# Kernel tuning notes

Hardware: AMD Instinct MI355X
Metric: run time of the kernel (lower is better)

Reference implementation:

```python
import sys
import jax, jax.numpy as jnp
import numpy as np

sys.setrecursionlimit(100000)

MARGIN = 200.0
SAME_MARGIN = 0.0
REL_MARGIN = MARGIN - SAME_MARGIN  # margin - same_margin


def km_algorithm(mp):
    """Faithful numpy port of the repo's recursive Kuhn-Munkres (host-side,
    exactly mirroring the original CPU round-trip). mp: (n, n) float64.
    Returns transport plan T with T[link[y], y] = 1/n for matched pairs."""
    n = mp.shape[0]
    link = np.full(n, -1, dtype=np.int64)
    lx = mp.max(axis=1).astype(np.float64).copy()
    ly = np.zeros(n, dtype=np.float64)
    st = {}

    def dfs(x):
        st['visx'][x] = True
        for y in range(n):
            if st['visy'][y]:
                continue
            tmp = lx[x] + ly[y] - mp[x, y]
            if abs(tmp) < 1e-5:
                st['visy'][y] = True
                if link[y] == -1 or dfs(link[y]):
                    link[y] = x
                    return True
            elif st['sla'][y] + 1e-5 > tmp:
                st['sla'][y] = tmp
        return False

    for x in range(n):
        st['sla'] = np.full(n, 1e10, dtype=np.float64)
        while True:
            st['visx'] = np.zeros(n, dtype=bool)
            st['visy'] = np.zeros(n, dtype=bool)
            if dfs(x):
                break
            d = st['sla'][~st['visy']].min()
            lx[st['visx']] -= d
            ly[st['visy']] += d
            st['sla'][~st['visy']] -= d
    T = np.zeros((n, n), dtype=np.float64)
    for i in range(n):
        if link[i] != -1:
            T[link[i], i] = 1.0 / n
    return T


def sim_label(l1, l2):
    # (n, n) float: 1 where labels equal
    return (l1[:, None] == l2[None, :]).astype(jnp.float32)


def ground_metric(f1, f2, sim):
    # pairwise squared euclidean distances: ||a||^2 - 2 a.b + ||b||^2
    sq1 = jnp.sum(f1 * f1, axis=1)[:, None]
    sq2 = jnp.sum(f2 * f2, axis=1)[None, :]
    d2 = sq1 - 2.0 * (f1 @ f2.T) + sq2
    hinge_gm = jnp.maximum(0.0, SAME_MARGIN + REL_MARGIN - d2)   # negative pairs
    same_gm = jnp.maximum(0.0, d2 - SAME_MARGIN)                 # positive pairs
    return sim * same_gm + (1.0 - sim) * hinge_gm                # mode='both'


def setup_inputs() -> dict:
    key = jax.random.key(0)
    k1, k2, k3, k4 = jax.random.split(key, 4)
    n, d = 128, 8192
    return {
        "inputs_batch1": jax.random.normal(k1, (n, d), dtype=jnp.float32),
        "inputs_batch2": jax.random.normal(k2, (n, d), dtype=jnp.float32),
        "targets_batch1": jax.random.randint(k3, (n,), 0, 16, dtype=jnp.int64) if jax.config.jax_enable_x64 else jax.random.randint(k3, (n,), 0, 16).astype(jnp.int32),
        "targets_batch2": jax.random.randint(k4, (n,), 0, 16, dtype=jnp.int64) if jax.config.jax_enable_x64 else jax.random.randint(k4, (n,), 0, 16).astype(jnp.int32),
    }


def reference(inputs_batch1, inputs_batch2, targets_batch1, targets_batch2):
    sim = sim_label(targets_batch1, targets_batch2)
    GM = ground_metric(inputs_batch1, inputs_batch2, sim)
    # host round-trip for KM assignment, as in the original module
    T = km_algorithm(np.asarray(jax.device_get(GM), dtype=np.float64))
    T = jnp.asarray(T, dtype=jnp.float32)
    loss = jnp.sum(GM * T)
    return loss
```

## Files before the change

### kernel.cpp

```cpp
#include <hip/hip_runtime.h>

#define N 128
#define DIM 8192
#define NN (N * N)
#define ZS 128
#define NW 16
#define GSTRIDE 130

__device__ __forceinline__ void wave_fence() {
    __threadfence_block();
    __builtin_amdgcn_wave_barrier();
}
__device__ __forceinline__ double embed_key(double v, int j) {
    long long b = __double_as_longlong(v);
    return __longlong_as_double((b & ~127LL) | (long long)j);
}

__global__ __launch_bounds__(256) void d2_partial(const float* __restrict__ A,
                                                  const float* __restrict__ B,
                                                  float* __restrict__ d2p) {
    __shared__ float As[64][68];
    __shared__ float Bk[64][68];
    const int tid = threadIdx.x;
    const int b = blockIdx.x;
    const int bi = b & 1, bj = (b >> 1) & 1, bz = b >> 2;
    const int row0 = bi * 64, col0 = bj * 64, k0 = bz * 64;

    #pragma unroll
    for (int s = 0; s < 4; ++s) {
        int e = tid + s * 256;
        int r = e >> 4, q = e & 15;
        *(float4*)&As[r][q * 4] = *(const float4*)&A[(row0 + r) * DIM + k0 + q * 4];
    }
    #pragma unroll
    for (int s = 0; s < 4; ++s) {
        int e = tid + s * 256;
        int c = e & 63, kq = e >> 6;
        float4 b4 = *(const float4*)&B[(col0 + c) * DIM + k0 + kq * 4];
        Bk[kq * 4 + 0][c] = b4.x;
        Bk[kq * 4 + 1][c] = b4.y;
        Bk[kq * 4 + 2][c] = b4.z;
        Bk[kq * 4 + 3][c] = b4.w;
    }
    __syncthreads();

    const int tx = tid & 15, ty = tid >> 4;
    float acc[4][4] = {};
    #pragma unroll
    for (int kk = 0; kk < 64; kk += 4) {
        float a[4][4], bb[4][4];
        #pragma unroll
        for (int i = 0; i < 4; ++i)
            *(float4*)a[i] = *(const float4*)&As[4 * ty + i][kk];
        #pragma unroll
        for (int q = 0; q < 4; ++q)
            *(float4*)bb[q] = *(const float4*)&Bk[kk + q][4 * tx];
        #pragma unroll
        for (int i = 0; i < 4; ++i)
            #pragma unroll
            for (int q = 0; q < 4; ++q) {
                float av = a[i][q];
                #pragma unroll
                for (int j = 0; j < 4; ++j) {
                    float d = av - bb[q][j];
                    acc[i][j] = fmaf(d, d, acc[i][j]);
                }
            }
    }
    float* dst = d2p + b * 4096;
    #pragma unroll
    for (int i = 0; i < 4; ++i)
        *(float4*)&dst[(4 * ty + i) * 64 + 4 * tx] = *(float4*)acc[i];
}

__global__ __launch_bounds__(256) void reduce_gm(const float* __restrict__ d2p,
                                                 const int* __restrict__ t1,
                                                 const int* __restrict__ t2,
                                                 float* __restrict__ gm,
                                                 int* __restrict__ flagarr) {
    __shared__ int bf;
    if (threadIdx.x == 0) bf = 0;
    __syncthreads();
    const int o = blockIdx.x * 256 + threadIdx.x;
    const int i = o >> 7, j = o & 127;
    const int tilebase = (((j >> 6) << 1) | (i >> 6)) * 4096;
    const int inner = (i & 63) * 64 + (j & 63);
    const float* p = d2p + tilebase + inner;
    float s0 = 0.f, s1 = 0.f, s2 = 0.f, s3 = 0.f, s4 = 0.f, s5 = 0.f, s6 = 0.f, s7 = 0.f;
    #pragma unroll
    for (int z = 0; z < ZS; z += 8) {
        s0 += p[(z + 0) * 16384]; s1 += p[(z + 1) * 16384];
        s2 += p[(z + 2) * 16384]; s3 += p[(z + 3) * 16384];
        s4 += p[(z + 4) * 16384]; s5 += p[(z + 5) * 16384];
        s6 += p[(z + 6) * 16384]; s7 += p[(z + 7) * 16384];
    }
    float s = ((s0 + s1) + (s2 + s3)) + ((s4 + s5) + (s6 + s7));
    const int l1 = t1[i], l2 = t2[j];
    const bool same = (l1 == l2);
    float g = same ? fmaxf(s, 0.f) : fmaxf(200.f - s, 0.f);
    gm[o] = g;
    bool bad = (!same && g > 0.f) || l1 < 0 || l1 > 63 || l2 < 0 || l2 > 63;
    unsigned long long m = __ballot(bad);
    if ((threadIdx.x & 63) == 0 && m) atomicOr(&bf, 1);
    __syncthreads();
    if (threadIdx.x == 0) flagarr[blockIdx.x] = bf;
}

__global__ __launch_bounds__(1024) void solve_kernel(const float* __restrict__ gm,
                                                     const int* __restrict__ flagarr,
                                                     const int* __restrict__ t1,
                                                     const int* __restrict__ t2,
                                                     float* __restrict__ out) {
    __shared__ float gml[N * GSTRIDE];
    __shared__ int lbl1[N], lbl2[N];
    __shared__ int rowlist[N], collist[N];
    __shared__ int rcnt[64], ccnt[64], rstart[65], cstart[65], rcur[64], ccur[64];
    __shared__ int tasks[65], bigtasks[65];
    __shared__ int ntasks_s, nbig_s, flag_s;
    __shared__ double totals[NW];
    __shared__ int claimw[NW][64];
    __shared__ double ub[N + 1], vbp[N + 1], minvb[N + 1];
    __shared__ int pb[N + 1], wayb[N + 1], usedb[N + 1];
    __shared__ double redv[NW];
    __shared__ int redi[NW];
    __shared__ double big_total;
    __shared__ int jfin_s;

    const int tid = threadIdx.x;
    if (tid < 64) { rcnt[tid] = 0; ccnt[tid] = 0; rcur[tid] = 0; ccur[tid] = 0; }
    if (tid == 0) { ntasks_s = 0; nbig_s = 0; flag_s = 0; big_total = 0.0; }
    if (tid < N)  { lbl1[tid] = t1[tid]; lbl2[tid] = t2[tid]; }
    __syncthreads();
    if (tid < 64 && flagarr[tid]) atomicOr(&flag_s, 1);
    if (tid < N) {
        atomicAdd(&rcnt[lbl1[tid] & 63], 1);
        atomicAdd(&ccnt[lbl2[tid] & 63], 1);
    }
    __syncthreads();
    if (tid < 64) {
        int rs_ = rcnt[tid], cs_ = ccnt[tid];
        #pragma unroll
        for (int o = 1; o < 64; o <<= 1) {
            int tr = __shfl_up(rs_, o, 64);
            int tc = __shfl_up(cs_, o, 64);
            if (tid >= o) { rs_ += tr; cs_ += tc; }
        }
        rstart[tid + 1] = rs_;
        cstart[tid + 1] = cs_;
        if (tid == 0) { rstart[0] = 0; cstart[0] = 0; }
        if (!flag_s) {
            int R = rcnt[tid], C = ccnt[tid];
            bool valid = (R > 0) && (C > 0);
            bool small = valid && (R <= 64) && (C <= 64);
            bool big   = valid && !small;
            unsigned long long ms = __ballot(small);
            unsigned long long mb = __ballot(big);
            if (small) tasks[__popcll(ms & ((1ull << tid) - 1))] = tid;
            if (big)   bigtasks[__popcll(mb & ((1ull << tid) - 1))] = tid;
            if (tid == 0) { ntasks_s = __popcll(ms); nbig_s = __popcll(mb); }
        } else if (tid == 0) { ntasks_s = 0; nbig_s = 1; bigtasks[0] = -1; }
    }
    __syncthreads();
    if (tid < N) {
        int l1 = lbl1[tid] & 63;
        int p = atomicAdd(&rcur[l1], 1);
        rowlist[rstart[l1] + p] = tid;
        int l2 = lbl2[tid] & 63;
        int q = atomicAdd(&ccur[l2], 1);
        collist[cstart[l2] + q] = tid;
    }
    __syncthreads();
    #pragma unroll
    for (int pch = 0; pch < 16; ++pch) {
        int e = tid + pch * 1024;
        int i = e >> 7, j = e & 127;
        gml[i * GSTRIDE + j] = gm[rowlist[i] * N + collist[j]];
    }
    __syncthreads();

    const int w = tid >> 6, lane = tid & 63;
    const int ntasks = ntasks_s;
    double acc = 0.0;

    for (int tk = w; tk < ntasks; tk += NW) {
        const int c = tasks[tk];
        const int Rn = rcnt[c], Cn = ccnt[c], rs = rstart[c], cs = cstart[c];
        const bool T  = (Rn > Cn);
        const int n_  = T ? Cn : Rn;
        const int m_  = T ? Rn : Cn;
        const int rstep = T ? 1 : GSTRIDE;
        const int cstep = T ? GSTRIDE : 1;
        const int rb00 = T ? cs : rs * GSTRIDE;
        const int ob00 = T ? rs * GSTRIDE : cs;
        int* clm = claimw[w];

        const bool cA = (lane < m_), rA = (lane < n_);
        const int myoff = ob00 + lane * cstep;
        const int myrb  = rb00 + lane * rstep;

        double u = 0.0;
        if (rA) {
            float mx = 0.f;
            int a = myrb + ob00;
            for (int j = 0; j < m_; ++j) { mx = fmaxf(mx, gml[a]); a += cstep; }
            u = -(double)mx;
        }
        double v = 1e30;
        {
            int a = rb00 + myoff;
            for (int i = 0; i < n_; ++i) {
                double ui = __shfl(u, i, 64);
                if (cA) v = fmin(v, -(double)gml[a] - ui);
                a += rstep;
            }
        }
        if (cA) clm[lane] = 0x7fffffff;
        wave_fence();
        int jc = -1;
        {
            int a = myrb + ob00;
            for (int j = 0; j < m_; ++j) {
                double vj = __shfl(v, j, 64);
                if (rA && jc < 0) {
                    double s = -(double)gml[a] - u - vj;
                    if (s < 1e-7) jc = j;
                }
                a += cstep;
            }
        }
        if (rA && jc >= 0) atomicMin(&clm[jc], lane);
        wave_fence();
        int p = -1;
        if (cA && clm[lane] != 0x7fffffff) p = clm[lane];
        bool rowm = (rA && jc >= 0 && clm[jc] == lane);

        for (int ir = 0; ir < n_; ++ir) {
            if (__shfl(rowm ? 1 : 0, ir, 64)) continue;
            double minv = 1e30, markD = -1.0, ent = -1.0;
            bool used = false; int way = -2;
            if (rA && lane == ir) ent = 0.0;
            double D = 0.0;
            int i0 = ir, jprev = -1;
            int guard = 2 * m_ + 8;
            while (guard-- > 0) {
                double ui = __shfl(u, i0, 64);
                int rb = rb00 + i0 * rstep;
                if (cA && !used) {
                    double cand = D - ui - (double)gml[rb + myoff] - v;
                    if (cand < minv) { minv = cand; way = jprev; }
                }
                double kd = (cA && !used) ? embed_key(minv, lane) : 1e30;
                #pragma unroll
                for (int o = 1; o < 64; o <<= 1) kd = fmin(kd, __shfl_xor(kd, o, 64));
                long long kb = __double_as_longlong(kd);
                int j1 = (int)(kb & 127);
                double Dn = __longlong_as_double(kb & ~127LL);
                if (Dn > 1e29) break;
                D = Dn;
                int i1 = __shfl(p, j1, 64);
                if (i1 < 0) {
                    int jj = j1;
                    while (true) {
                        int wp = __shfl(way, jj, 64);
                        int pn = (wp < 0) ? ir : __shfl(p, wp, 64);
                        if (cA && lane == jj) p = pn;
                        if (wp < 0) break;
                        jj = wp;
                    }
                    if (rA && lane == ir) rowm = true;
                    break;
                }
                if (cA && lane == j1) { used = true; markD = D; }
                if (rA && lane == i1) ent = D;
                jprev = j1; i0 = i1;
            }
            if (rA && ent   >= 0.0) u += D - ent;
            if (cA && markD >= 0.0) v -= D - markD;
        }

        double val = 0.0;
        if (cA && p >= 0) val = (double)gml[rb00 + p * rstep + myoff];
        #pragma unroll
        for (int o = 1; o < 64; o <<= 1) val += __shfl_xor(val, o, 64);
        acc += val;
    }
    if (lane == 0) totals[w] = acc;
    __syncthreads();

    const int nbig = nbig_s;
    for (int bt = 0; bt < nbig; ++bt) {
        const int c = bigtasks[bt];
        int Rn, Cn, rs, cs;
        if (c < 0) { Rn = N; Cn = N; rs = 0; cs = 0; }
        else { Rn = rcnt[c]; Cn = ccnt[c]; rs = rstart[c]; cs = cstart[c]; }
        const bool T = (Rn > Cn);
        const int n_ = T ? Cn : Rn, m_ = T ? Rn : Cn;
        const int rstep = T ? 1 : GSTRIDE;
        const int cstep = T ? GSTRIDE : 1;
        const int rb00 = T ? cs : rs * GSTRIDE;
        const int ob00 = T ? rs * GSTRIDE : cs;
        auto cost = [&](int i, int j) -> double {
            return -(double)gml[rb00 + i * rstep + ob00 + j * cstep];
        };
        for (int x = tid; x <= m_; x += 1024) { vbp[x] = 0.0; pb[x] = 0; }
        for (int x = tid; x <= n_; x += 1024) { ub[x] = 0.0; }
        __syncthreads();
        for (int i = 1; i <= n_; ++i) {
            if (tid == 0) pb[0] = i;
            for (int x = tid; x <= m_; x += 1024) { minvb[x] = 1e300; usedb[x] = 0; }
            __syncthreads();
            int j0 = 0;
            int guard = 2 * m_ + 8;
            while (guard-- > 0) {
                if (tid == 0) usedb[j0] = 1;
                __syncthreads();
                const int i0 = pb[j0];
                double dl = 1e300; int jl = 0;
                if (tid < m_) {
                    int j = tid + 1;
                    if (!usedb[j]) {
                        double cur = cost(i0 - 1, j - 1) - ub[i0] - vbp[j];
                        if (cur < minvb[j]) { minvb[j] = cur; wayb[j] = j0; }
                        dl = minvb[j]; jl = j;
                    }
                }
                double rv = dl; int ri = jl;
                #pragma unroll
                for (int o = 32; o > 0; o >>= 1) {
                    double ov = __shfl_down(rv, o, 64);
                    int oi2 = __shfl_down(ri, o, 64);
                    if (ov < rv) { rv = ov; ri = oi2; }
                }
                if ((tid & 63) == 0) { redv[tid >> 6] = rv; redi[tid >> 6] = ri; }
                __syncthreads();
                if (tid == 0) {
                    double bd = 1e300; int bj = 0;
                    for (int q = 0; q < NW; ++q) if (redv[q] < bd) { bd = redv[q]; bj = redi[q]; }
                    redv[0] = bd; redi[0] = bj;
                }
                __syncthreads();
                const double delta = redv[0];
                const int j1 = redi[0];
                if (tid < m_) {
                    int j = tid + 1;
                    if (usedb[j]) { ub[pb[j]] += delta; vbp[j] -= delta; }
                    else          { minvb[j] -= delta; }
                }
                if (tid == 0) ub[pb[0]] += delta;
                __syncthreads();
                j0 = j1;
                if (pb[j0] == 0) break;
            }
            if (tid == 0) jfin_s = j0;
            __syncthreads();
            if (tid == 0) {
                int jj = jfin_s;
                while (jj) { int jp = wayb[jj]; pb[jj] = pb[jp]; jj = jp; }
            }
            __syncthreads();
        }
        double bl = 0.0;
        if (tid < m_) { int j = tid + 1; if (pb[j] != 0) bl = -cost(pb[j] - 1, j - 1); }
        #pragma unroll
        for (int o = 32; o > 0; o >>= 1) bl += __shfl_down(bl, o, 64);
        if ((tid & 63) == 0) redv[tid >> 6] = bl;
        __syncthreads();
        if (tid == 0) { double s = 0; for (int q = 0; q < NW; ++q) s += redv[q]; big_total += s; }
        __syncthreads();
    }

    if (tid == 0) {
        double s = big_total;
        for (int i = 0; i < NW; ++i) s += totals[i];
        out[0] = (float)(s / (double)N);
    }
}

extern "C" void kernel_launch(void* const* d_in, const int* in_sizes, int n_in,
                              void* d_out, int out_size, void* d_ws, size_t ws_size,
                              hipStream_t stream) {
    const float* A  = (const float*)d_in[0];
    const float* B  = (const float*)d_in[1];
    const int*   t1 = (const int*)d_in[2];
    const int*   t2 = (const int*)d_in[3];
    float* out = (float*)d_out;
    float* d2p = (float*)d_ws;
    float* gm  = (float*)d_ws + ZS * 4 * 4096;
    int*   flagarr = (int*)(gm + NN);

    d2_partial<<<ZS * 4, 256, 0, stream>>>(A, B, d2p);
    reduce_gm<<<64, 256, 0, stream>>>(d2p, t1, t2, gm, flagarr);
    solve_kernel<<<1, 1024, 0, stream>>>(gm, flagarr, t1, t2, out);
}
```

Baseline: 92.40 us.

## Split z-reduction across more threads and write label-permuted GM from reduce kernel

The reduce kernel now uses 1024 threads per block and splits the 128-slice partial-sum reduction four ways, combining the pieces through shared memory. This raises memory-level parallelism in the global reads. It also computes each row's and column's position in label-sorted order and writes GM directly in that permuted layout. The single-block solve kernel then loads it with contiguous float4 reads instead of a gather through row and column lists. The cost is that every reduce block redundantly recomputes the label counts and sorted positions, including an O(n) counting loop per thread.

```diff
diff --git a/kernel.cpp b/kernel.cpp
--- a/kernel.cpp
+++ b/kernel.cpp
@@ -73,48 +73,89 @@
         *(float4*)&dst[(4 * ty + i) * 64 + 4 * tx] = *(float4*)acc[i];
 }
 
-__global__ __launch_bounds__(256) void reduce_gm(const float* __restrict__ d2p,
-                                                 const int* __restrict__ t1,
-                                                 const int* __restrict__ t2,
-                                                 float* __restrict__ gm,
-                                                 int* __restrict__ flagarr) {
+__global__ __launch_bounds__(1024) void reduce_gm(const float* __restrict__ d2p,
+                                                  const int* __restrict__ t1,
+                                                  const int* __restrict__ t2,
+                                                  float* __restrict__ gmp,
+                                                  int* __restrict__ flagarr) {
+    __shared__ int l1o[N], l2o[N], l1c[N], l2c[N];
+    __shared__ int rc[64], cc[64], rst[64], cst[64];
+    __shared__ int rpos[N], cpos[N];
+    __shared__ float psum[3][256];
     __shared__ int bf;
-    if (threadIdx.x == 0) bf = 0;
-    __syncthreads();
-    const int o = blockIdx.x * 256 + threadIdx.x;
+    const int tid = threadIdx.x;
+    if (tid == 0) bf = 0;
+    if (tid < 64) { rc[tid] = 0; cc[tid] = 0; }
+    if (tid < N) {
+        int a = t1[tid], b = t2[tid];
+        l1o[tid] = a; l2o[tid] = b; l1c[tid] = a & 63; l2c[tid] = b & 63;
+    }
+    __syncthreads();
+    if (tid < N) {
+        atomicAdd(&rc[l1c[tid]], 1);
+        atomicAdd(&cc[l2c[tid]], 1);
+        if (l1o[tid] < 0 || l1o[tid] > 63 || l2o[tid] < 0 || l2o[tid] > 63) atomicOr(&bf, 1);
+    }
+    __syncthreads();
+    if (tid < 64) {
+        int rs_ = rc[tid], cs_ = cc[tid];
+        #pragma unroll
+        for (int o = 1; o < 64; o <<= 1) {
+            int tr = __shfl_up(rs_, o, 64);
+            int tc = __shfl_up(cs_, o, 64);
+            if (tid >= o) { rs_ += tr; cs_ += tc; }
+        }
+        rst[tid] = rs_ - rc[tid];
+        cst[tid] = cs_ - cc[tid];
+    }
+    __syncthreads();
+    if (tid < N) {
+        int cr = 0, L = l1c[tid];
+        int cq = 0, M = l2c[tid];
+        for (int k = 0; k < tid; ++k) {
+            cr += (l1c[k] == L);
+            cq += (l2c[k] == M);
+        }
+        rpos[tid] = rst[L] + cr;
+        cpos[tid] = cst[M] + cq;
+    }
+    __syncthreads();
+
+    const int oo = tid & 255, zq = tid >> 8;
+    const int o = blockIdx.x * 256 + oo;
     const int i = o >> 7, j = o & 127;
-    const int tilebase = (((j >> 6) << 1) | (i >> 6)) * 4096;
-    const int inner = (i & 63) * 64 + (j & 63);
-    const float* p = d2p + tilebase + inner;
+    const int tb = (((j >> 6) << 1) | (i >> 6)) * 4096;
+    const float* p = d2p + tb + (i & 63) * 64 + (j & 63) + zq * 32 * 16384;
     float s0 = 0.f, s1 = 0.f, s2 = 0.f, s3 = 0.f, s4 = 0.f, s5 = 0.f, s6 = 0.f, s7 = 0.f;
     #pragma unroll
-    for (int z = 0; z < ZS; z += 8) {
+    for (int z = 0; z < 32; z += 8) {
         s0 += p[(z + 0) * 16384]; s1 += p[(z + 1) * 16384];
         s2 += p[(z + 2) * 16384]; s3 += p[(z + 3) * 16384];
         s4 += p[(z + 4) * 16384]; s5 += p[(z + 5) * 16384];
         s6 += p[(z + 6) * 16384]; s7 += p[(z + 7) * 16384];
     }
     float s = ((s0 + s1) + (s2 + s3)) + ((s4 + s5) + (s6 + s7));
-    const int l1 = t1[i], l2 = t2[j];
-    const bool same = (l1 == l2);
-    float g = same ? fmaxf(s, 0.f) : fmaxf(200.f - s, 0.f);
-    gm[o] = g;
-    bool bad = (!same && g > 0.f) || l1 < 0 || l1 > 63 || l2 < 0 || l2 > 63;
-    unsigned long long m = __ballot(bad);
-    if ((threadIdx.x & 63) == 0 && m) atomicOr(&bf, 1);
-    __syncthreads();
-    if (threadIdx.x == 0) flagarr[blockIdx.x] = bf;
-}
-
-__global__ __launch_bounds__(1024) void solve_kernel(const float* __restrict__ gm,
+    if (zq) psum[zq - 1][oo] = s;
+    __syncthreads();
+    if (zq == 0) {
+        s += psum[0][oo] + psum[1][oo] + psum[2][oo];
+        const bool same = (l1o[i] == l2o[j]);
+        float g = same ? fmaxf(s, 0.f) : fmaxf(200.f - s, 0.f);
+        gmp[rpos[i] * N + cpos[j]] = g;
+        if (!same && g > 0.f) atomicOr(&bf, 1);
+    }
+    __syncthreads();
+    if (tid == 0) flagarr[blockIdx.x] = bf;
+}
+
+__global__ __launch_bounds__(1024) void solve_kernel(const float* __restrict__ gmp,
                                                      const int* __restrict__ flagarr,
                                                      const int* __restrict__ t1,
                                                      const int* __restrict__ t2,
                                                      float* __restrict__ out) {
     __shared__ float gml[N * GSTRIDE];
     __shared__ int lbl1[N], lbl2[N];
-    __shared__ int rowlist[N], collist[N];
-    __shared__ int rcnt[64], ccnt[64], rstart[65], cstart[65], rcur[64], ccur[64];
+    __shared__ int rcnt[64], ccnt[64], rstart[65], cstart[65];
     __shared__ int tasks[65], bigtasks[65];
     __shared__ int ntasks_s, nbig_s, flag_s;
     __shared__ double totals[NW];
@@ -127,7 +168,15 @@
     __shared__ int jfin_s;
 
     const int tid = threadIdx.x;
-    if (tid < 64) { rcnt[tid] = 0; ccnt[tid] = 0; rcur[tid] = 0; ccur[tid] = 0; }
+    #pragma unroll
+    for (int pch = 0; pch < 4; ++pch) {
+        int e = (tid + pch * 1024) * 4;
+        int i = e >> 7, j = e & 127;
+        float4 v4 = *(const float4*)&gmp[e];
+        *(float2*)&gml[i * GSTRIDE + j]     = make_float2(v4.x, v4.y);
+        *(float2*)&gml[i * GSTRIDE + j + 2] = make_float2(v4.z, v4.w);
+    }
+    if (tid < 64) { rcnt[tid] = 0; ccnt[tid] = 0; }
     if (tid == 0) { ntasks_s = 0; nbig_s = 0; flag_s = 0; big_total = 0.0; }
     if (tid < N)  { lbl1[tid] = t1[tid]; lbl2[tid] = t2[tid]; }
     __syncthreads();
@@ -159,22 +208,6 @@
             if (big)   bigtasks[__popcll(mb & ((1ull << tid) - 1))] = tid;
             if (tid == 0) { ntasks_s = __popcll(ms); nbig_s = __popcll(mb); }
         } else if (tid == 0) { ntasks_s = 0; nbig_s = 1; bigtasks[0] = -1; }
-    }
-    __syncthreads();
-    if (tid < N) {
-        int l1 = lbl1[tid] & 63;
-        int p = atomicAdd(&rcur[l1], 1);
-        rowlist[rstart[l1] + p] = tid;
-        int l2 = lbl2[tid] & 63;
-        int q = atomicAdd(&ccur[l2], 1);
-        collist[cstart[l2] + q] = tid;
-    }
-    __syncthreads();
-    #pragma unroll
-    for (int pch = 0; pch < 16; ++pch) {
-        int e = tid + pch * 1024;
-        int i = e >> 7, j = e & 127;
-        gml[i * GSTRIDE + j] = gm[rowlist[i] * N + collist[j]];
     }
     __syncthreads();
 
@@ -385,10 +418,10 @@
     const int*   t2 = (const int*)d_in[3];
     float* out = (float*)d_out;
     float* d2p = (float*)d_ws;
-    float* gm  = (float*)d_ws + ZS * 4 * 4096;
-    int*   flagarr = (int*)(gm + NN);
+    float* gmp = (float*)d_ws + ZS * 4 * 4096;
+    int*   flagarr = (int*)(gmp + NN);
 
     d2_partial<<<ZS * 4, 256, 0, stream>>>(A, B, d2p);
-    reduce_gm<<<64, 256, 0, stream>>>(d2p, t1, t2, gm, flagarr);
-    solve_kernel<<<1, 1024, 0, stream>>>(gm, flagarr, t1, t2, out);
-}
+    reduce_gm<<<64, 1024, 0, stream>>>(d2p, t1, t2, gmp, flagarr);
+    solve_kernel<<<1, 1024, 0, stream>>>(gmp, flagarr, t1, t2, out);
+}
```

Result: no change. 91.78 us (-0.7%).

## Fuse three kernels into one persistent kernel with software grid barriers

Applied to the files above, without the earlier changes.

Merges the distance-partial, reduction and assignment-solve kernels into a single 512-block launch synchronized by spin-wait grid barriers on a control struct in workspace. The small per-label assignment tasks are spread across 4 blocks of 256 threads instead of one 1024-thread block, and the partial sums are combined with a global atomic. This removes two launch gaps but relies on all 512 blocks being co-resident (launch_bounds 256,2). It also runs the large-case Hungarian solve with only 256 threads, and the ready/MAGIC handshake may be fragile across repeated calls.

```diff
diff --git a/kernel.cpp b/kernel.cpp
--- a/kernel.cpp
+++ b/kernel.cpp
@@ -4,8 +4,14 @@
 #define DIM 8192
 #define NN (N * N)
 #define ZS 128
-#define NW 16
+#define NBLK 512
 #define GSTRIDE 130
+#define MAGIC 0x5ca1ab1e
+
+struct Ctl {
+    double acc;
+    int cnt, gen, ready, flag, done, pad;
+};
 
 __device__ __forceinline__ void wave_fence() {
     __threadfence_block();
@@ -16,175 +22,201 @@
     return __longlong_as_double((b & ~127LL) | (long long)j);
 }
 
-__global__ __launch_bounds__(256) void d2_partial(const float* __restrict__ A,
-                                                  const float* __restrict__ B,
-                                                  float* __restrict__ d2p) {
-    __shared__ float As[64][68];
-    __shared__ float Bk[64][68];
+__device__ __forceinline__ void grid_barrier(Ctl* ctl) {
+    __threadfence();
+    __syncthreads();
+    if (threadIdx.x == 0) {
+        long t = 0;
+        while (__hip_atomic_load(&ctl->ready, __ATOMIC_ACQUIRE, __HIP_MEMORY_SCOPE_AGENT) != MAGIC
+               && ++t < 400000000L) __builtin_amdgcn_s_sleep(1);
+        int g = __hip_atomic_load(&ctl->gen, __ATOMIC_ACQUIRE, __HIP_MEMORY_SCOPE_AGENT);
+        int a = __hip_atomic_fetch_add(&ctl->cnt, 1, __ATOMIC_ACQ_REL, __HIP_MEMORY_SCOPE_AGENT);
+        if (a == NBLK - 1) {
+            __hip_atomic_store(&ctl->cnt, 0, __ATOMIC_RELAXED, __HIP_MEMORY_SCOPE_AGENT);
+            __hip_atomic_store(&ctl->gen, g + 1, __ATOMIC_RELEASE, __HIP_MEMORY_SCOPE_AGENT);
+        } else {
+            t = 0;
+            while (__hip_atomic_load(&ctl->gen, __ATOMIC_ACQUIRE, __HIP_MEMORY_SCOPE_AGENT) == g
+                   && ++t < 400000000L) __builtin_amdgcn_s_sleep(1);
+        }
+    }
+    __syncthreads();
+    __threadfence();
+}
+
+union SH {
+    struct { float As[64][68]; float Bk[64][68]; } a;
+    struct {
+        float gml[N * GSTRIDE];
+        int lbl1[N], lbl2[N];
+        int rowlist[N], collist[N];
+        int rcnt[64], ccnt[64], rstart[65], cstart[65], rcur[64], ccur[64];
+        int tasks[65], bigtasks[65];
+        int ntasks, nbig, flag;
+        double totals[4];
+        int claimw[4][64];
+        double ub[N + 1], vbp[N + 1], minvb[N + 1];
+        int pb[N + 1], wayb[N + 1], usedb[N + 1];
+        double redv[4]; int redi[4];
+        double big_total; int jfin;
+    } s;
+};
+
+__global__ __launch_bounds__(256, 2) void mvp_fused(const float* __restrict__ A,
+                                                    const float* __restrict__ B,
+                                                    const int* __restrict__ t1,
+                                                    const int* __restrict__ t2,
+                                                    float* __restrict__ d2p,
+                                                    float* __restrict__ gm,
+                                                    Ctl* ctl,
+                                                    float* __restrict__ out) {
+    __shared__ SH sh;
     const int tid = threadIdx.x;
-    const int b = blockIdx.x;
-    const int bi = b & 1, bj = (b >> 1) & 1, bz = b >> 2;
-    const int row0 = bi * 64, col0 = bj * 64, k0 = bz * 64;
-
-    #pragma unroll
-    for (int s = 0; s < 4; ++s) {
-        int e = tid + s * 256;
-        int r = e >> 4, q = e & 15;
-        *(float4*)&As[r][q * 4] = *(const float4*)&A[(row0 + r) * DIM + k0 + q * 4];
-    }
-    #pragma unroll
-    for (int s = 0; s < 4; ++s) {
-        int e = tid + s * 256;
-        int c = e & 63, kq = e >> 6;
-        float4 b4 = *(const float4*)&B[(col0 + c) * DIM + k0 + kq * 4];
-        Bk[kq * 4 + 0][c] = b4.x;
-        Bk[kq * 4 + 1][c] = b4.y;
-        Bk[kq * 4 + 2][c] = b4.z;
-        Bk[kq * 4 + 3][c] = b4.w;
-    }
-    __syncthreads();
-
-    const int tx = tid & 15, ty = tid >> 4;
-    float acc[4][4] = {};
-    #pragma unroll
-    for (int kk = 0; kk < 64; kk += 4) {
-        float a[4][4], bb[4][4];
+    const int blk = blockIdx.x;
+
+    if (blk == 0 && tid == 0) {
+        ctl->acc = 0.0; ctl->flag = 0; ctl->done = 0;
+        __hip_atomic_store(&ctl->cnt, 0, __ATOMIC_RELAXED, __HIP_MEMORY_SCOPE_AGENT);
+        __hip_atomic_store(&ctl->gen, 0, __ATOMIC_RELAXED, __HIP_MEMORY_SCOPE_AGENT);
+        __threadfence();
+        __hip_atomic_store(&ctl->ready, MAGIC, __ATOMIC_RELEASE, __HIP_MEMORY_SCOPE_AGENT);
+    }
+    {
+        const int bi = blk & 1, bj = (blk >> 1) & 1, bz = blk >> 2;
+        const int row0 = bi * 64, col0 = bj * 64, k0 = bz * 64;
+        #pragma unroll
+        for (int s = 0; s < 4; ++s) {
+            int e = tid + s * 256;
+            int r = e >> 4, q = e & 15;
+            *(float4*)&sh.a.As[r][q * 4] = *(const float4*)&A[(row0 + r) * DIM + k0 + q * 4];
+        }
+        #pragma unroll
+        for (int s = 0; s < 4; ++s) {
+            int e = tid + s * 256;
+            int c = e & 63, kq = e >> 6;
+            float4 b4 = *(const float4*)&B[(col0 + c) * DIM + k0 + kq * 4];
+            sh.a.Bk[kq * 4 + 0][c] = b4.x;
+            sh.a.Bk[kq * 4 + 1][c] = b4.y;
+            sh.a.Bk[kq * 4 + 2][c] = b4.z;
+            sh.a.Bk[kq * 4 + 3][c] = b4.w;
+        }
+        __syncthreads();
+        const int tx = tid & 15, ty = tid >> 4;
+        float acc4[4][4] = {};
+        #pragma unroll
+        for (int kk = 0; kk < 64; kk += 4) {
+            float a[4][4], bb[4][4];
+            #pragma unroll
+            for (int i = 0; i < 4; ++i)
+                *(float4*)a[i] = *(const float4*)&sh.a.As[4 * ty + i][kk];
+            #pragma unroll
+            for (int q = 0; q < 4; ++q)
+                *(float4*)bb[q] = *(const float4*)&sh.a.Bk[kk + q][4 * tx];
+            #pragma unroll
+            for (int i = 0; i < 4; ++i)
+                #pragma unroll
+                for (int q = 0; q < 4; ++q) {
+                    float av = a[i][q];
+                    #pragma unroll
+                    for (int j = 0; j < 4; ++j) {
+                        float d = av - bb[q][j];
+                        acc4[i][j] = fmaf(d, d, acc4[i][j]);
+                    }
+                }
+        }
+        float* dst = d2p + blk * 4096;
         #pragma unroll
         for (int i = 0; i < 4; ++i)
-            *(float4*)a[i] = *(const float4*)&As[4 * ty + i][kk];
-        #pragma unroll
-        for (int q = 0; q < 4; ++q)
-            *(float4*)bb[q] = *(const float4*)&Bk[kk + q][4 * tx];
-        #pragma unroll
-        for (int i = 0; i < 4; ++i)
-            #pragma unroll
-            for (int q = 0; q < 4; ++q) {
-                float av = a[i][q];
-                #pragma unroll
-                for (int j = 0; j < 4; ++j) {
-                    float d = av - bb[q][j];
-                    acc[i][j] = fmaf(d, d, acc[i][j]);
-                }
-            }
-    }
-    float* dst = d2p + b * 4096;
-    #pragma unroll
-    for (int i = 0; i < 4; ++i)
-        *(float4*)&dst[(4 * ty + i) * 64 + 4 * tx] = *(float4*)acc[i];
-}
-
-__global__ __launch_bounds__(256) void reduce_gm(const float* __restrict__ d2p,
-                                                 const int* __restrict__ t1,
-                                                 const int* __restrict__ t2,
-                                                 float* __restrict__ gm,
-                                                 int* __restrict__ flagarr) {
-    __shared__ int bf;
-    if (threadIdx.x == 0) bf = 0;
-    __syncthreads();
-    const int o = blockIdx.x * 256 + threadIdx.x;
-    const int i = o >> 7, j = o & 127;
-    const int tilebase = (((j >> 6) << 1) | (i >> 6)) * 4096;
-    const int inner = (i & 63) * 64 + (j & 63);
-    const float* p = d2p + tilebase + inner;
-    float s0 = 0.f, s1 = 0.f, s2 = 0.f, s3 = 0.f, s4 = 0.f, s5 = 0.f, s6 = 0.f, s7 = 0.f;
-    #pragma unroll
-    for (int z = 0; z < ZS; z += 8) {
-        s0 += p[(z + 0) * 16384]; s1 += p[(z + 1) * 16384];
-        s2 += p[(z + 2) * 16384]; s3 += p[(z + 3) * 16384];
-        s4 += p[(z + 4) * 16384]; s5 += p[(z + 5) * 16384];
-        s6 += p[(z + 6) * 16384]; s7 += p[(z + 7) * 16384];
-    }
-    float s = ((s0 + s1) + (s2 + s3)) + ((s4 + s5) + (s6 + s7));
-    const int l1 = t1[i], l2 = t2[j];
-    const bool same = (l1 == l2);
-    float g = same ? fmaxf(s, 0.f) : fmaxf(200.f - s, 0.f);
-    gm[o] = g;
-    bool bad = (!same && g > 0.f) || l1 < 0 || l1 > 63 || l2 < 0 || l2 > 63;
-    unsigned long long m = __ballot(bad);
-    if ((threadIdx.x & 63) == 0 && m) atomicOr(&bf, 1);
-    __syncthreads();
-    if (threadIdx.x == 0) flagarr[blockIdx.x] = bf;
-}
-
-__global__ __launch_bounds__(1024) void solve_kernel(const float* __restrict__ gm,
-                                                     const int* __restrict__ flagarr,
-                                                     const int* __restrict__ t1,
-                                                     const int* __restrict__ t2,
-                                                     float* __restrict__ out) {
-    __shared__ float gml[N * GSTRIDE];
-    __shared__ int lbl1[N], lbl2[N];
-    __shared__ int rowlist[N], collist[N];
-    __shared__ int rcnt[64], ccnt[64], rstart[65], cstart[65], rcur[64], ccur[64];
-    __shared__ int tasks[65], bigtasks[65];
-    __shared__ int ntasks_s, nbig_s, flag_s;
-    __shared__ double totals[NW];
-    __shared__ int claimw[NW][64];
-    __shared__ double ub[N + 1], vbp[N + 1], minvb[N + 1];
-    __shared__ int pb[N + 1], wayb[N + 1], usedb[N + 1];
-    __shared__ double redv[NW];
-    __shared__ int redi[NW];
-    __shared__ double big_total;
-    __shared__ int jfin_s;
-
-    const int tid = threadIdx.x;
-    if (tid < 64) { rcnt[tid] = 0; ccnt[tid] = 0; rcur[tid] = 0; ccur[tid] = 0; }
-    if (tid == 0) { ntasks_s = 0; nbig_s = 0; flag_s = 0; big_total = 0.0; }
-    if (tid < N)  { lbl1[tid] = t1[tid]; lbl2[tid] = t2[tid]; }
-    __syncthreads();
-    if (tid < 64 && flagarr[tid]) atomicOr(&flag_s, 1);
+            *(float4*)&dst[(4 * ty + i) * 64 + 4 * tx] = *(float4*)acc4[i];
+    }
+    grid_barrier(ctl);
+
+    if (blk < 64) {
+        const int o = blk * 256 + tid;
+        const int i = o >> 7, j = o & 127;
+        const int tb = (((j >> 6) << 1) | (i >> 6)) * 4096;
+        const float* p = d2p + tb + (i & 63) * 64 + (j & 63);
+        float s16[16];
+        #pragma unroll
+        for (int q = 0; q < 16; ++q) s16[q] = 0.f;
+        #pragma unroll
+        for (int z = 0; z < ZS; z += 16)
+            #pragma unroll
+            for (int q = 0; q < 16; ++q) s16[q] += p[(z + q) * 16384];
+        #pragma unroll
+        for (int st = 8; st > 0; st >>= 1)
+            #pragma unroll
+            for (int q = 0; q < 8; ++q) if (q < st) s16[q] += s16[q + st];
+        float s = s16[0];
+        const int l1 = t1[i], l2 = t2[j];
+        const bool same = (l1 == l2);
+        float g = same ? fmaxf(s, 0.f) : fmaxf(200.f - s, 0.f);
+        gm[o] = g;
+        bool bad = (!same && g > 0.f) || l1 < 0 || l1 > 63 || l2 < 0 || l2 > 63;
+        unsigned long long m = __ballot(bad);
+        if ((tid & 63) == 0 && m) atomicOr(&ctl->flag, 1);
+    }
+    grid_barrier(ctl);
+
+    if (blk >= 4) return;
+
+    if (tid < 64) { sh.s.rcnt[tid] = 0; sh.s.ccnt[tid] = 0; sh.s.rcur[tid] = 0; sh.s.ccur[tid] = 0; }
+    if (tid == 0) { sh.s.ntasks = 0; sh.s.nbig = 0; sh.s.big_total = 0.0; sh.s.flag = ctl->flag; }
+    if (tid < N)  { sh.s.lbl1[tid] = t1[tid]; sh.s.lbl2[tid] = t2[tid]; }
+    __syncthreads();
     if (tid < N) {
-        atomicAdd(&rcnt[lbl1[tid] & 63], 1);
-        atomicAdd(&ccnt[lbl2[tid] & 63], 1);
+        atomicAdd(&sh.s.rcnt[sh.s.lbl1[tid] & 63], 1);
+        atomicAdd(&sh.s.ccnt[sh.s.lbl2[tid] & 63], 1);
     }
     __syncthreads();
     if (tid < 64) {
-        int rs_ = rcnt[tid], cs_ = ccnt[tid];
+        int rs_ = sh.s.rcnt[tid], cs_ = sh.s.ccnt[tid];
         #pragma unroll
         for (int o = 1; o < 64; o <<= 1) {
             int tr = __shfl_up(rs_, o, 64);
             int tc = __shfl_up(cs_, o, 64);
             if (tid >= o) { rs_ += tr; cs_ += tc; }
         }
-        rstart[tid + 1] = rs_;
-        cstart[tid + 1] = cs_;
-        if (tid == 0) { rstart[0] = 0; cstart[0] = 0; }
-        if (!flag_s) {
-            int R = rcnt[tid], C = ccnt[tid];
+        sh.s.rstart[tid + 1] = rs_;
+        sh.s.cstart[tid + 1] = cs_;
+        if (tid == 0) { sh.s.rstart[0] = 0; sh.s.cstart[0] = 0; }
+        if (!sh.s.flag) {
+            int R = sh.s.rcnt[tid], C = sh.s.ccnt[tid];
             bool valid = (R > 0) && (C > 0);
             bool small = valid && (R <= 64) && (C <= 64);
             bool big   = valid && !small;
             unsigned long long ms = __ballot(small);
             unsigned long long mb = __ballot(big);
-            if (small) tasks[__popcll(ms & ((1ull << tid) - 1))] = tid;
-            if (big)   bigtasks[__popcll(mb & ((1ull << tid) - 1))] = tid;
-            if (tid == 0) { ntasks_s = __popcll(ms); nbig_s = __popcll(mb); }
-        } else if (tid == 0) { ntasks_s = 0; nbig_s = 1; bigtasks[0] = -1; }
+            if (small) sh.s.tasks[__popcll(ms & ((1ull << tid) - 1))] = tid;
+            if (big)   sh.s.bigtasks[__popcll(mb & ((1ull << tid) - 1))] = tid;
+            if (tid == 0) { sh.s.ntasks = __popcll(ms); sh.s.nbig = __popcll(mb); }
+        } else if (tid == 0) { sh.s.ntasks = 0; sh.s.nbig = 1; sh.s.bigtasks[0] = -1; }
     }
     __syncthreads();
     if (tid < N) {
-        int l1 = lbl1[tid] & 63;
-        int p = atomicAdd(&rcur[l1], 1);
-        rowlist[rstart[l1] + p] = tid;
-        int l2 = lbl2[tid] & 63;
-        int q = atomicAdd(&ccur[l2], 1);
-        collist[cstart[l2] + q] = tid;
-    }
-    __syncthreads();
-    #pragma unroll
-    for (int pch = 0; pch < 16; ++pch) {
-        int e = tid + pch * 1024;
+        int l1 = sh.s.lbl1[tid] & 63;
+        int p = atomicAdd(&sh.s.rcur[l1], 1);
+        sh.s.rowlist[sh.s.rstart[l1] + p] = tid;
+        int l2 = sh.s.lbl2[tid] & 63;
+        int q = atomicAdd(&sh.s.ccur[l2], 1);
+        sh.s.collist[sh.s.cstart[l2] + q] = tid;
+    }
+    __syncthreads();
+    for (int e = tid; e < NN; e += 256) {
         int i = e >> 7, j = e & 127;
-        gml[i * GSTRIDE + j] = gm[rowlist[i] * N + collist[j]];
-    }
-    __syncthreads();
-
-    const int w = tid >> 6, lane = tid & 63;
-    const int ntasks = ntasks_s;
+        sh.s.gml[i * GSTRIDE + j] = gm[sh.s.rowlist[i] * N + sh.s.collist[j]];
+    }
+    __syncthreads();
+
+    const int lw = tid >> 6, lane = tid & 63;
+    const int ntasks = sh.s.ntasks;
     double acc = 0.0;
-
-    for (int tk = w; tk < ntasks; tk += NW) {
-        const int c = tasks[tk];
-        const int Rn = rcnt[c], Cn = ccnt[c], rs = rstart[c], cs = cstart[c];
+    float* gml = sh.s.gml;
+
+    for (int tk = blk * 4 + lw; tk < ntasks; tk += 16) {
+        const int c = sh.s.tasks[tk];
+        const int Rn = sh.s.rcnt[c], Cn = sh.s.ccnt[c];
+        const int rs = sh.s.rstart[c], cs = sh.s.cstart[c];
         const bool T  = (Rn > Cn);
         const int n_  = T ? Cn : Rn;
         const int m_  = T ? Rn : Cn;
@@ -192,7 +224,7 @@
         const int cstep = T ? GSTRIDE : 1;
         const int rb00 = T ? cs : rs * GSTRIDE;
         const int ob00 = T ? rs * GSTRIDE : cs;
-        int* clm = claimw[w];
+        int* clm = sh.s.claimw[lw];
 
         const bool cA = (lane < m_), rA = (lane < n_);
         const int myoff = ob00 + lane * cstep;
@@ -284,95 +316,105 @@
         for (int o = 1; o < 64; o <<= 1) val += __shfl_xor(val, o, 64);
         acc += val;
     }
-    if (lane == 0) totals[w] = acc;
-    __syncthreads();
-
-    const int nbig = nbig_s;
-    for (int bt = 0; bt < nbig; ++bt) {
-        const int c = bigtasks[bt];
-        int Rn, Cn, rs, cs;
-        if (c < 0) { Rn = N; Cn = N; rs = 0; cs = 0; }
-        else { Rn = rcnt[c]; Cn = ccnt[c]; rs = rstart[c]; cs = cstart[c]; }
-        const bool T = (Rn > Cn);
-        const int n_ = T ? Cn : Rn, m_ = T ? Rn : Cn;
-        const int rstep = T ? 1 : GSTRIDE;
-        const int cstep = T ? GSTRIDE : 1;
-        const int rb00 = T ? cs : rs * GSTRIDE;
-        const int ob00 = T ? rs * GSTRIDE : cs;
-        auto cost = [&](int i, int j) -> double {
-            return -(double)gml[rb00 + i * rstep + ob00 + j * cstep];
-        };
-        for (int x = tid; x <= m_; x += 1024) { vbp[x] = 0.0; pb[x] = 0; }
-        for (int x = tid; x <= n_; x += 1024) { ub[x] = 0.0; }
-        __syncthreads();
-        for (int i = 1; i <= n_; ++i) {
-            if (tid == 0) pb[0] = i;
-            for (int x = tid; x <= m_; x += 1024) { minvb[x] = 1e300; usedb[x] = 0; }
+    if (lane == 0) sh.s.totals[lw] = acc;
+    __syncthreads();
+
+    if (blk == 0) {
+        const int nbig = sh.s.nbig;
+        for (int bt = 0; bt < nbig; ++bt) {
+            const int c = sh.s.bigtasks[bt];
+            int Rn, Cn, rs, cs;
+            if (c < 0) { Rn = N; Cn = N; rs = 0; cs = 0; }
+            else { Rn = sh.s.rcnt[c]; Cn = sh.s.ccnt[c]; rs = sh.s.rstart[c]; cs = sh.s.cstart[c]; }
+            const bool T = (Rn > Cn);
+            const int n_ = T ? Cn : Rn, m_ = T ? Rn : Cn;
+            const int rstep = T ? 1 : GSTRIDE;
+            const int cstep = T ? GSTRIDE : 1;
+            const int rb00 = T ? cs : rs * GSTRIDE;
+            const int ob00 = T ? rs * GSTRIDE : cs;
+            auto cost = [&](int i, int j) -> double {
+                return -(double)gml[rb00 + i * rstep + ob00 + j * cstep];
+            };
+            for (int x = tid; x <= m_; x += 256) { sh.s.vbp[x] = 0.0; sh.s.pb[x] = 0; }
+            for (int x = tid; x <= n_; x += 256) { sh.s.ub[x] = 0.0; }
             __syncthreads();
-            int j0 = 0;
-            int guard = 2 * m_ + 8;
-            while (guard-- > 0) {
-                if (tid == 0) usedb[j0] = 1;
+            for (int i = 1; i <= n_; ++i) {
+                if (tid == 0) sh.s.pb[0] = i;
+                for (int x = tid; x <= m_; x += 256) { sh.s.minvb[x] = 1e300; sh.s.usedb[x] = 0; }
                 __syncthreads();
-                const int i0 = pb[j0];
-                double dl = 1e300; int jl = 0;
-                if (tid < m_) {
-                    int j = tid + 1;
-                    if (!usedb[j]) {
-                        double cur = cost(i0 - 1, j - 1) - ub[i0] - vbp[j];
-                        if (cur < minvb[j]) { minvb[j] = cur; wayb[j] = j0; }
-                        dl = minvb[j]; jl = j;
-                    }
-                }
-                double rv = dl; int ri = jl;
-                #pragma unroll
-                for (int o = 32; o > 0; o >>= 1) {
-                    double ov = __shfl_down(rv, o, 64);
-                    int oi2 = __shfl_down(ri, o, 64);
-                    if (ov < rv) { rv = ov; ri = oi2; }
-                }
-                if ((tid & 63) == 0) { redv[tid >> 6] = rv; redi[tid >> 6] = ri; }
+                int j0 = 0;
+                int guard = 2 * m_ + 8;
+                while (guard-- > 0) {
+                    if (tid == 0) sh.s.usedb[j0] = 1;
+                    __syncthreads();
+                    const int i0 = sh.s.pb[j0];
+                    double dl = 1e300; int jl = 0;
+                    for (int j = tid + 1; j <= m_; j += 256) {
+                        if (!sh.s.usedb[j]) {
+                            double cur = cost(i0 - 1, j - 1) - sh.s.ub[i0] - sh.s.vbp[j];
+                            if (cur < sh.s.minvb[j]) { sh.s.minvb[j] = cur; sh.s.wayb[j] = j0; }
+                            if (sh.s.minvb[j] < dl) { dl = sh.s.minvb[j]; jl = j; }
+                        }
+                    }
+                    double rv = dl; int ri = jl;
+                    #pragma unroll
+                    for (int o = 32; o > 0; o >>= 1) {
+                        double ov = __shfl_down(rv, o, 64);
+                        int oi2 = __shfl_down(ri, o, 64);
+                        if (ov < rv) { rv = ov; ri = oi2; }
+                    }
+                    if ((tid & 63) == 0) { sh.s.redv[tid >> 6] = rv; sh.s.redi[tid >> 6] = ri; }
+                    __syncthreads();
+                    if (tid == 0) {
+                        double bd = 1e300; int bj = 0;
+                        for (int q = 0; q < 4; ++q) if (sh.s.redv[q] < bd) { bd = sh.s.redv[q]; bj = sh.s.redi[q]; }
+                        sh.s.redv[0] = bd; sh.s.redi[0] = bj;
+                    }
+                    __syncthreads();
+                    const double delta = sh.s.redv[0];
+                    const int j1 = sh.s.redi[0];
+                    for (int j = tid + 1; j <= m_; j += 256) {
+                        if (sh.s.usedb[j]) { sh.s.ub[sh.s.pb[j]] += delta; sh.s.vbp[j] -= delta; }
+                        else               { sh.s.minvb[j] -= delta; }
+                    }
+                    if (tid == 0) sh.s.ub[sh.s.pb[0]] += delta;
+                    __syncthreads();
+                    j0 = j1;
+                    if (sh.s.pb[j0] == 0) break;
+                }
+                if (tid == 0) {
+                    int jj = j0;
+                    while (jj) { int jp = sh.s.wayb[jj]; sh.s.pb[jj] = sh.s.pb[jp]; jj = jp; }
+                }
                 __syncthreads();
-                if (tid == 0) {
-                    double bd = 1e300; int bj = 0;
-                    for (int q = 0; q < NW; ++q) if (redv[q] < bd) { bd = redv[q]; bj = redi[q]; }
-                    redv[0] = bd; redi[0] = bj;
-                }
-                __syncthreads();
-                const double delta = redv[0];
-                const int j1 = redi[0];
-                if (tid < m_) {
-                    int j = tid + 1;
-                    if (usedb[j]) { ub[pb[j]] += delta; vbp[j] -= delta; }
-                    else          { minvb[j] -= delta; }
-                }
-                if (tid == 0) ub[pb[0]] += delta;
-                __syncthreads();
-                j0 = j1;
-                if (pb[j0] == 0) break;
             }
-            if (tid == 0) jfin_s = j0;
+            double bl = 0.0;
+            for (int j = tid + 1; j <= m_; j += 256)
+                if (sh.s.pb[j] != 0) bl += -cost(sh.s.pb[j] - 1, j - 1);
+            #pragma unroll
+            for (int o = 32; o > 0; o >>= 1) bl += __shfl_down(bl, o, 64);
+            if ((tid & 63) == 0) sh.s.redv[tid >> 6] = bl;
             __syncthreads();
             if (tid == 0) {
-                int jj = jfin_s;
-                while (jj) { int jp = wayb[jj]; pb[jj] = pb[jp]; jj = jp; }
+                double s = 0;
+                for (int q = 0; q < 4; ++q) s += sh.s.redv[q];
+                sh.s.big_total += s;
             }
             __syncthreads();
         }
-        double bl = 0.0;
-        if (tid < m_) { int j = tid + 1; if (pb[j] != 0) bl = -cost(pb[j] - 1, j - 1); }
-        #pragma unroll
-        for (int o = 32; o > 0; o >>= 1) bl += __shfl_down(bl, o, 64);
-        if ((tid & 63) == 0) redv[tid >> 6] = bl;
-        __syncthreads();
-        if (tid == 0) { double s = 0; for (int q = 0; q < NW; ++q) s += redv[q]; big_total += s; }
-        __syncthreads();
     }
 
     if (tid == 0) {
-        double s = big_total;
-        for (int i = 0; i < NW; ++i) s += totals[i];
-        out[0] = (float)(s / (double)N);
+        double part = sh.s.totals[0] + sh.s.totals[1] + sh.s.totals[2] + sh.s.totals[3];
+        if (blk == 0) part += sh.s.big_total;
+        atomicAdd(&ctl->acc, part);
+        __threadfence();
+        int old = __hip_atomic_fetch_add(&ctl->done, 1, __ATOMIC_ACQ_REL, __HIP_MEMORY_SCOPE_AGENT);
+        if (old == 3) {
+            __threadfence();
+            double s = *(volatile double*)&ctl->acc;
+            out[0] = (float)(s / (double)N);
+        }
     }
 }
 
@@ -385,10 +427,8 @@
     const int*   t2 = (const int*)d_in[3];
     float* out = (float*)d_out;
     float* d2p = (float*)d_ws;
-    float* gm  = (float*)d_ws + ZS * 4 * 4096;
-    int*   flagarr = (int*)(gm + NN);
-
-    d2_partial<<<ZS * 4, 256, 0, stream>>>(A, B, d2p);
-    reduce_gm<<<64, 256, 0, stream>>>(d2p, t1, t2, gm, flagarr);
-    solve_kernel<<<1, 1024, 0, stream>>>(gm, flagarr, t1, t2, out);
+    float* gm  = d2p + NBLK * 4096;
+    Ctl*   ctl = (Ctl*)(gm + NN);
+
+    mvp_fused<<<NBLK, 256, 0, stream>>>(A, B, t1, t2, d2p, gm, ctl, out);
 }
```

Result: slower. 358.2 us (+287.6%).

## Halve K-slice depth to double d2 blocks and split reduction across threads

Applied to the files above, without the earlier changes.

Each d2_partial block now covers 32 K-elements instead of 64, so 1024 blocks are launched instead of 512, which raises occupancy across the GPU's compute units. The reduce kernel now launches 128 blocks, with two threads per output each summing half of the 256 partial slices and combining through shared memory. The solver reads 128 flags instead of 64. The cost is twice as much partial-sum traffic to write and read back, 16 MB instead of 8 MB, plus a larger reduction.

```diff
diff --git a/kernel.cpp b/kernel.cpp
--- a/kernel.cpp
+++ b/kernel.cpp
@@ -3,7 +3,7 @@
 #define N 128
 #define DIM 8192
 #define NN (N * N)
-#define ZS 128
+#define NSLICE 1024
 #define NW 16
 #define GSTRIDE 130
 
@@ -19,23 +19,23 @@
 __global__ __launch_bounds__(256) void d2_partial(const float* __restrict__ A,
                                                   const float* __restrict__ B,
                                                   float* __restrict__ d2p) {
-    __shared__ float As[64][68];
-    __shared__ float Bk[64][68];
+    __shared__ float As[64][36];
+    __shared__ float Bk[32][68];
     const int tid = threadIdx.x;
     const int b = blockIdx.x;
     const int bi = b & 1, bj = (b >> 1) & 1, bz = b >> 2;
-    const int row0 = bi * 64, col0 = bj * 64, k0 = bz * 64;
-
-    #pragma unroll
-    for (int s = 0; s < 4; ++s) {
+    const int row0 = bi * 64, col0 = bj * 64, k0 = bz * 32;
+
+    #pragma unroll
+    for (int s = 0; s < 2; ++s) {
         int e = tid + s * 256;
-        int r = e >> 4, q = e & 15;
+        int r = e >> 3, q = e & 7;
         *(float4*)&As[r][q * 4] = *(const float4*)&A[(row0 + r) * DIM + k0 + q * 4];
     }
     #pragma unroll
-    for (int s = 0; s < 4; ++s) {
+    for (int s = 0; s < 2; ++s) {
         int e = tid + s * 256;
-        int c = e & 63, kq = e >> 6;
+        int kq = e & 7, c = e >> 3;
         float4 b4 = *(const float4*)&B[(col0 + c) * DIM + k0 + kq * 4];
         Bk[kq * 4 + 0][c] = b4.x;
         Bk[kq * 4 + 1][c] = b4.y;
@@ -47,7 +47,7 @@
     const int tx = tid & 15, ty = tid >> 4;
     float acc[4][4] = {};
     #pragma unroll
-    for (int kk = 0; kk < 64; kk += 4) {
+    for (int kk = 0; kk < 32; kk += 4) {
         float a[4][4], bb[4][4];
         #pragma unroll
         for (int i = 0; i < 4; ++i)
@@ -78,32 +78,41 @@
                                                  const int* __restrict__ t2,
                                                  float* __restrict__ gm,
                                                  int* __restrict__ flagarr) {
+    __shared__ float psum[128];
     __shared__ int bf;
-    if (threadIdx.x == 0) bf = 0;
-    __syncthreads();
-    const int o = blockIdx.x * 256 + threadIdx.x;
+    const int tid = threadIdx.x;
+    if (tid == 0) bf = 0;
+    const int oo = tid & 127, zq = tid >> 7;
+    const int o = blockIdx.x * 128 + oo;
     const int i = o >> 7, j = o & 127;
-    const int tilebase = (((j >> 6) << 1) | (i >> 6)) * 4096;
-    const int inner = (i & 63) * 64 + (j & 63);
-    const float* p = d2p + tilebase + inner;
-    float s0 = 0.f, s1 = 0.f, s2 = 0.f, s3 = 0.f, s4 = 0.f, s5 = 0.f, s6 = 0.f, s7 = 0.f;
-    #pragma unroll
-    for (int z = 0; z < ZS; z += 8) {
-        s0 += p[(z + 0) * 16384]; s1 += p[(z + 1) * 16384];
-        s2 += p[(z + 2) * 16384]; s3 += p[(z + 3) * 16384];
-        s4 += p[(z + 4) * 16384]; s5 += p[(z + 5) * 16384];
-        s6 += p[(z + 6) * 16384]; s7 += p[(z + 7) * 16384];
-    }
-    float s = ((s0 + s1) + (s2 + s3)) + ((s4 + s5) + (s6 + s7));
-    const int l1 = t1[i], l2 = t2[j];
-    const bool same = (l1 == l2);
-    float g = same ? fmaxf(s, 0.f) : fmaxf(200.f - s, 0.f);
-    gm[o] = g;
-    bool bad = (!same && g > 0.f) || l1 < 0 || l1 > 63 || l2 < 0 || l2 > 63;
-    unsigned long long m = __ballot(bad);
-    if ((threadIdx.x & 63) == 0 && m) atomicOr(&bf, 1);
-    __syncthreads();
-    if (threadIdx.x == 0) flagarr[blockIdx.x] = bf;
+    const int tb = (((j >> 6) << 1) | (i >> 6)) * 4096;
+    const float* p = d2p + tb + (i & 63) * 64 + (j & 63) + zq * (128 * 16384);
+    float s16[16];
+    #pragma unroll
+    for (int q = 0; q < 16; ++q) s16[q] = 0.f;
+    #pragma unroll
+    for (int z = 0; z < 128; z += 16)
+        #pragma unroll
+        for (int q = 0; q < 16; ++q) s16[q] += p[(z + q) * 16384];
+    #pragma unroll
+    for (int st = 8; st > 0; st >>= 1)
+        #pragma unroll
+        for (int q = 0; q < 8; ++q) if (q < st) s16[q] += s16[q + st];
+    float s = s16[0];
+    if (zq) psum[oo] = s;
+    __syncthreads();
+    if (!zq) {
+        s += psum[oo];
+        const int l1 = t1[i], l2 = t2[j];
+        const bool same = (l1 == l2);
+        float g = same ? fmaxf(s, 0.f) : fmaxf(200.f - s, 0.f);
+        gm[o] = g;
+        bool bad = (!same && g > 0.f) || l1 < 0 || l1 > 63 || l2 < 0 || l2 > 63;
+        unsigned long long m = __ballot(bad);
+        if ((tid & 63) == 0 && m) atomicOr(&bf, 1);
+    }
+    __syncthreads();
+    if (tid == 0) flagarr[blockIdx.x] = bf;
 }
 
 __global__ __launch_bounds__(1024) void solve_kernel(const float* __restrict__ gm,
@@ -131,7 +140,7 @@
     if (tid == 0) { ntasks_s = 0; nbig_s = 0; flag_s = 0; big_total = 0.0; }
     if (tid < N)  { lbl1[tid] = t1[tid]; lbl2[tid] = t2[tid]; }
     __syncthreads();
-    if (tid < 64 && flagarr[tid]) atomicOr(&flag_s, 1);
+    if (tid < 128 && flagarr[tid]) atomicOr(&flag_s, 1);
     if (tid < N) {
         atomicAdd(&rcnt[lbl1[tid] & 63], 1);
         atomicAdd(&ccnt[lbl2[tid] & 63], 1);
@@ -385,10 +394,10 @@
     const int*   t2 = (const int*)d_in[3];
     float* out = (float*)d_out;
     float* d2p = (float*)d_ws;
-    float* gm  = (float*)d_ws + ZS * 4 * 4096;
+    float* gm  = d2p + NSLICE * 4096;
     int*   flagarr = (int*)(gm + NN);
 
-    d2_partial<<<ZS * 4, 256, 0, stream>>>(A, B, d2p);
-    reduce_gm<<<64, 256, 0, stream>>>(d2p, t1, t2, gm, flagarr);
+    d2_partial<<<NSLICE, 256, 0, stream>>>(A, B, d2p);
+    reduce_gm<<<128, 256, 0, stream>>>(d2p, t1, t2, gm, flagarr);
     solve_kernel<<<1, 1024, 0, stream>>>(gm, flagarr, t1, t2, out);
 }
```

Result: slower. 119.6 us (+29.5%).
